# Performance work log

Hardware: AMD Instinct MI355X
Metric: run time of the kernel (lower is better)

## Reference

```python
import jax, jax.numpy as jnp
import numpy as np

EPS = 1e-12


def sage_pool_conv(x, src, dst, W_pool, b_pool, W_self, W_neigh, b, num_nodes):
    """DGL SAGEConv with aggregator_type='pool':
    h_neigh[v] = max_{u in N(v)} relu(x[u] @ W_pool + b_pool)
    out[v] = x[v] @ W_self + h_neigh[v] @ W_neigh + b
    Zero-in-degree nodes get h_neigh = 0 (DGL fills max over empty set with 0).
    """
    m = jax.nn.relu(x[src] @ W_pool + b_pool)            # [E, F] gathered + transformed
    agg = jax.ops.segment_max(m, dst, num_segments=num_nodes)  # [N, F], -inf where no neighbors
    agg = jnp.where(jnp.isneginf(agg), 0.0, agg)
    return x @ W_self + agg @ W_neigh + b


def l2norm_relu(h):
    # F.normalize(h, p=2, dim=1, eps=1e-12) then relu
    n = jnp.maximum(jnp.linalg.norm(h, axis=1, keepdims=True), EPS)
    return jax.nn.relu(h / n)


def setup_inputs() -> dict:
    key = jax.random.key(0)
    N, E = 50000, 1600000
    IN, HID, OUT = 128, 128, 128
    ks = jax.random.split(key, 16)
    s = 0.05
    return {
        "x": jax.random.normal(ks[0], (N, IN), dtype=jnp.float32),
        "src": jax.random.randint(ks[1], (E,), 0, N, dtype=jnp.int32),
        "dst": jax.random.randint(ks[2], (E,), 0, N, dtype=jnp.int32),
        "W_pool1": jax.random.normal(ks[3], (IN, IN), dtype=jnp.float32) * s,
        "b_pool1": jnp.zeros((IN,), dtype=jnp.float32),
        "W_self1": jax.random.normal(ks[4], (IN, HID), dtype=jnp.float32) * s,
        "W_neigh1": jax.random.normal(ks[5], (IN, HID), dtype=jnp.float32) * s,
        "b1": jnp.zeros((HID,), dtype=jnp.float32),
        "W_pool2": jax.random.normal(ks[6], (HID, HID), dtype=jnp.float32) * s,
        "b_pool2": jnp.zeros((HID,), dtype=jnp.float32),
        "W_self2": jax.random.normal(ks[7], (HID, OUT), dtype=jnp.float32) * s,
        "W_neigh2": jax.random.normal(ks[8], (HID, OUT), dtype=jnp.float32) * s,
        "b2": jnp.zeros((OUT,), dtype=jnp.float32),
    }


def reference(x, src, dst, W_pool1, b_pool1, W_self1, W_neigh1, b1,
              W_pool2, b_pool2, W_self2, W_neigh2, b2):
    N = x.shape[0]
    h = sage_pool_conv(x, src, dst, W_pool1, b_pool1, W_self1, W_neigh1, b1, N)
    h = l2norm_relu(h)
    # dropout_1 is re-assigned in the original forward but never applied -> no dropout
    h = sage_pool_conv(h, src, dst, W_pool2, b_pool2, W_self2, W_neigh2, b2, N)
    h = l2norm_relu(h)
    return h
```

## Files before the change

### kernel.cpp

```cpp
#include <hip/hip_runtime.h>
#include <hip/hip_bf16.h>

#define NF 128
#define TILE_B 8192
#define NSLAB 8
#define SLAB_SHIFT 13
#define CSR_CAP 15360

typedef __attribute__((ext_vector_type(8))) short bf8;
typedef __attribute__((ext_vector_type(4))) float f4;
typedef unsigned short u16x8 __attribute__((ext_vector_type(8)));

static __device__ __forceinline__ unsigned short f2bf(float f) {
  unsigned u = __builtin_bit_cast(unsigned, f);
  u = u + 0x7FFF + ((u >> 16) & 1);
  return (unsigned short)(u >> 16);
}

static __device__ __forceinline__ uint4 pkmax4(uint4 a, uint4 b) {
  u16x8 x = __builtin_bit_cast(u16x8, a);
  u16x8 y = __builtin_bit_cast(u16x8, b);
  u16x8 m = __builtin_elementwise_max(x, y);
  return __builtin_bit_cast(uint4, m);
}

static __device__ __forceinline__ uint4 shflxor4(uint4 a, int m) {
  uint4 r;
  r.x = (unsigned)__shfl_xor((int)a.x, m, 64);
  r.y = (unsigned)__shfl_xor((int)a.y, m, 64);
  r.z = (unsigned)__shfl_xor((int)a.z, m, 64);
  r.w = (unsigned)__shfl_xor((int)a.w, m, 64);
  return r;
}


__global__ __launch_bounds__(256) void k_prep(
    const float* __restrict__ x, unsigned short* __restrict__ Xb, long long nelX,
    const int* __restrict__ dst, int* __restrict__ bcnt, int E, int gTile,
    const float* W0, const float* W1, const float* W2,
    const float* W3, const float* W4, const float* W5,
    unsigned short* __restrict__ Wpack) {
  __shared__ int h[256];
  int b = blockIdx.x, tid = threadIdx.x;

  long long i = ((long long)b * 256 + tid) * 8;
  if (i + 8 <= nelX) {
    float4 a = *(const float4*)(x + i);
    float4 c = *(const float4*)(x + i + 4);
    uint4 o;
    o.x = f2bf(a.x) | ((unsigned)f2bf(a.y) << 16);
    o.y = f2bf(a.z) | ((unsigned)f2bf(a.w) << 16);
    o.z = f2bf(c.x) | ((unsigned)f2bf(c.y) << 16);
    o.w = f2bf(c.z) | ((unsigned)f2bf(c.w) << 16);
    *(uint4*)(Xb + i) = o;
  }

  if (b < gTile) {
    h[tid] = 0;
    __syncthreads();
    int t0 = b * TILE_B;
    int tend = min(E, t0 + TILE_B);
    for (int k = t0 + tid; k < tend; k += 256) atomicAdd(&h[dst[k] >> 8], 1);
    __syncthreads();
    if (h[tid] > 0) atomicAdd(&bcnt[tid], h[tid]);
  } else if (b < gTile + 48) {
    int gid = (b - gTile) * 256 + tid;
    int m = gid >> 11;
    int u = gid & 2047;
    const float* W = (m == 0) ? W0 : (m == 1) ? W1 : (m == 2) ? W2
                   : (m == 3) ? W3 : (m == 4) ? W4 : W5;
    int l = u & 63, c = u >> 6;
    int kk = c & 3, t = c >> 2;
    int kb = kk * 32 + ((l >> 4) << 3);
    int n = t * 16 + (l & 15);
    unsigned short* o = Wpack + (size_t)m * 2048 * 8 + (size_t)u * 8;
    #pragma unroll
    for (int j = 0; j < 8; ++j) o[j] = f2bf(W[(size_t)(kb + j) * NF + n]);
  }
}


__global__ __launch_bounds__(256) void k_binB(const int* __restrict__ src,
                                              const int* __restrict__ dst,
                                              const int* __restrict__ bcnt,
                                              int* __restrict__ gcur,
                                              unsigned* __restrict__ tmp, int E) {
  __shared__ int h[256], hs[256], gb[256], lc[256], bo[256];
  __shared__ unsigned sorted[TILE_B];
  int tid = threadIdx.x;
  int t0 = blockIdx.x * TILE_B;
  int tcnt = min(E - t0, TILE_B);
  if (tcnt <= 0) return;

  int bv = bcnt[tid];
  hs[tid] = bv;
  __syncthreads();
  for (int d = 1; d < 256; d <<= 1) {
    int t = (tid >= d) ? hs[tid - d] : 0;
    __syncthreads();
    hs[tid] += t;
    __syncthreads();
  }
  bo[tid] = hs[tid] - bv;
  h[tid] = 0;
  __syncthreads();

  for (int i = tid; i < tcnt; i += 256) atomicAdd(&h[dst[t0 + i] >> 8], 1);
  __syncthreads();
  int v = h[tid];
  hs[tid] = v;
  __syncthreads();
  for (int d = 1; d < 256; d <<= 1) {
    int t = (tid >= d) ? hs[tid - d] : 0;
    __syncthreads();
    hs[tid] += t;
    __syncthreads();
  }
  lc[tid] = 0;
  gb[tid] = bo[tid] + ((v > 0) ? atomicAdd(&gcur[tid], v) : 0);
  __syncthreads();
  for (int i = tid; i < tcnt; i += 256) {
    int d = dst[t0 + i];
    unsigned s = (unsigned)src[t0 + i];
    int b = d >> 8;
    int p = (hs[b] - h[b]) + atomicAdd(&lc[b], 1);
    sorted[p] = ((unsigned)b << 24) | (s << 8) | (unsigned)(d & 255);
  }
  __syncthreads();
  for (int i = tid; i < tcnt; i += 256) {
    unsigned ev = sorted[i];
    int b = ev >> 24;
    tmp[gb[b] + (i - (hs[b] - h[b]))] = ev & 0xFFFFFFu;
  }
}


__global__ __launch_bounds__(256) void k_binC(const unsigned* __restrict__ tmp,
                                              const int* __restrict__ bcnt,
                                              int* __restrict__ off,
                                              unsigned short* __restrict__ esrc,
                                              int N, int E) {
  __shared__ int pre[256 * NSLAB];
  __shared__ int lc2[256 * NSLAB];
  __shared__ int s256[256];
  __shared__ int bo[256];
  __shared__ int csr[CSR_CAP];
  int tid = threadIdx.x;
  int b = blockIdx.x;
  int base = b << 8;

  int bv = bcnt[tid];
  s256[tid] = bv;
  __syncthreads();
  for (int d = 1; d < 256; d <<= 1) {
    int t = (tid >= d) ? s256[tid - d] : 0;
    __syncthreads();
    s256[tid] += t;
    __syncthreads();
  }
  bo[tid] = s256[tid] - bv;
  for (int k = tid; k < 256 * NSLAB; k += 256) { pre[k] = 0; lc2[k] = 0; }
  __syncthreads();

  int beg = bo[b];
  int cnt = bcnt[b];
  int end = beg + cnt;

  for (int i = beg + tid; i < end; i += 256) {
    unsigned e = tmp[i];
    int key = ((e & 255) << 3) | (e >> (8 + SLAB_SHIFT));
    atomicAdd(&pre[key], 1);
  }
  __syncthreads();
  {
    int sum = 0;
    #pragma unroll
    for (int j = 0; j < NSLAB; ++j) {
      int v = pre[tid * NSLAB + j];
      pre[tid * NSLAB + j] = sum;
      sum += v;
    }
    s256[tid] = sum;
    __syncthreads();
    for (int d = 1; d < 256; d <<= 1) {
      int t = (tid >= d) ? s256[tid - d] : 0;
      __syncthreads();
      s256[tid] += t;
      __syncthreads();
    }
    int segbase = s256[tid] - sum;
    #pragma unroll
    for (int j = 0; j < NSLAB; ++j) pre[tid * NSLAB + j] += segbase;
  }
  __syncthreads();

  if (base + tid < N) off[base + tid] = beg + pre[tid * NSLAB];
  if (b == 0 && tid == 0) off[N] = E;

  if (cnt <= CSR_CAP) {
    for (int i = beg + tid; i < end; i += 256) {
      unsigned e = tmp[i];
      int key = ((e & 255) << 3) | (e >> (8 + SLAB_SHIFT));
      int p = pre[key] + atomicAdd(&lc2[key], 1);
      csr[p] = (int)(e >> 8);
    }
    __syncthreads();
    for (int i = tid; i < cnt; i += 256) esrc[beg + i] = (unsigned short)csr[i];
  } else {
    for (int i = beg + tid; i < end; i += 256) {
      unsigned e = tmp[i];
      int key = ((e & 255) << 3) | (e >> (8 + SLAB_SHIFT));
      int p = pre[key] + atomicAdd(&lc2[key], 1);
      esrc[beg + p] = (unsigned short)(e >> 8);
    }
  }
}


__global__ __launch_bounds__(512) void k_gemm_pool(
    const unsigned short* __restrict__ A, const unsigned short* __restrict__ P,
    const float* __restrict__ bias, unsigned short* __restrict__ Yout, int M) {
  __shared__ __align__(16) char smem[32768 + 8 * 4096];
  int tid = threadIdx.x, w = tid >> 6, lane = tid & 63;
  int r0 = lane & 15, g = lane >> 4;

  {
    uint4* S = (uint4*)smem;
    const uint4* Pv = (const uint4*)P;
    for (int t = tid; t < 2048; t += 512) S[t] = Pv[t];
  }
  float bb[8];
  #pragma unroll
  for (int t = 0; t < 8; ++t) bb[t] = bias[t * 16 + r0];
  __syncthreads();

  const bf8* Wl = (const bf8*)smem;
  char* myst = smem + 32768 + w * 4096;

  int T = (M + 15) >> 4;
  int stride = gridDim.x * 8;
  for (int t0i = blockIdx.x * 8 + w; t0i < T; t0i += stride) {
    int rowbase = t0i * 16;
    int arow = min(rowbase + r0, M - 1);

    f4 acc[8];
    #pragma unroll
    for (int t = 0; t < 8; ++t) acc[t] = (f4){0.f, 0.f, 0.f, 0.f};

    const bf8* Ar = (const bf8*)(A + (size_t)arow * NF);
    #pragma unroll
    for (int kk = 0; kk < 4; ++kk) {
      bf8 a = Ar[kk * 4 + g];
      #pragma unroll
      for (int t = 0; t < 8; ++t)
        acc[t] = __builtin_amdgcn_mfma_f32_16x16x32_bf16(a, Wl[(t * 4 + kk) * 64 + lane], acc[t], 0, 0, 0);
    }

    unsigned short* So = (unsigned short*)myst;
    #pragma unroll
    for (int i = 0; i < 4; ++i)
      #pragma unroll
      for (int t = 0; t < 8; ++t)
        So[(g * 4 + i) * NF + t * 16 + r0] = f2bf(fmaxf(acc[t][i] + bb[t], 0.f));
    uint4* Og = (uint4*)(Yout + (size_t)rowbase * NF);
    const uint4* Sv = (const uint4*)myst;
    int maxc = min(16, M - rowbase) * 16;
    #pragma unroll
    for (int k = 0; k < 4; ++k) {
      int c = lane + k * 64;
      if (c < maxc) Og[c] = Sv[c];
    }
  }
}


template <int OUT_MODE>
__global__ __launch_bounds__(256) void k_gemm_dual(
    const unsigned short* __restrict__ A0, const unsigned short* __restrict__ P0,
    const unsigned short* __restrict__ A1, const unsigned short* __restrict__ P1,
    const float* __restrict__ bias, void* __restrict__ Cout, int M) {
  constexpr int STG = (OUT_MODE == 2) ? 8192 : 4096;
  __shared__ __align__(16) char smem[4 * STG];
  int tid = threadIdx.x, w = tid >> 6, lane = tid & 63;
  int r0 = lane & 15, g = lane >> 4;
  int rowbase = (blockIdx.x * 4 + w) * 16;
  if (rowbase >= M) return;
  int arow = min(rowbase + r0, M - 1);
  char* myst = smem + w * STG;

  f4 acc[8];
  #pragma unroll
  for (int t = 0; t < 8; ++t) acc[t] = (f4){0.f, 0.f, 0.f, 0.f};

  #pragma unroll
  for (int mat = 0; mat < 2; ++mat) {
    const unsigned short* A = (mat == 0) ? A0 : A1;
    const bf8* Pp = (const bf8*)((mat == 0) ? P0 : P1);
    const bf8* Ar = (const bf8*)(A + (size_t)arow * NF);
    #pragma unroll
    for (int kk = 0; kk < 4; ++kk) {
      bf8 a = Ar[kk * 4 + g];
      #pragma unroll
      for (int t = 0; t < 8; ++t)
        acc[t] = __builtin_amdgcn_mfma_f32_16x16x32_bf16(a, Pp[(t * 4 + kk) * 64 + lane], acc[t], 0, 0, 0);
    }
  }

  float bb[8];
  #pragma unroll
  for (int t = 0; t < 8; ++t) bb[t] = bias[t * 16 + r0];

  float val[8][4];
  #pragma unroll
  for (int t = 0; t < 8; ++t)
    #pragma unroll
    for (int i = 0; i < 4; ++i) val[t][i] = acc[t][i] + bb[t];

  float ss[4] = {0.f, 0.f, 0.f, 0.f};
  #pragma unroll
  for (int i = 0; i < 4; ++i)
    #pragma unroll
    for (int t = 0; t < 8; ++t) ss[i] += val[t][i] * val[t][i];
  #pragma unroll
  for (int d = 1; d < 16; d <<= 1)
    #pragma unroll
    for (int i = 0; i < 4; ++i) ss[i] += __shfl_xor(ss[i], d, 64);
  float inv[4];
  #pragma unroll
  for (int i = 0; i < 4; ++i) inv[i] = 1.f / fmaxf(sqrtf(ss[i]), 1e-12f);

  int maxrows = min(16, M - rowbase);
  if (OUT_MODE == 2) {
    float* So = (float*)myst;
    #pragma unroll
    for (int i = 0; i < 4; ++i)
      #pragma unroll
      for (int t = 0; t < 8; ++t)
        So[(g * 4 + i) * NF + t * 16 + r0] = fmaxf(val[t][i] * inv[i], 0.f);
    uint4* Og = (uint4*)((float*)Cout + (size_t)rowbase * NF);
    const uint4* Sv = (const uint4*)myst;
    int maxc = maxrows * 32;
    #pragma unroll
    for (int k = 0; k < 8; ++k) {
      int c = lane + k * 64;
      if (c < maxc) Og[c] = Sv[c];
    }
  } else {
    unsigned short* So = (unsigned short*)myst;
    #pragma unroll
    for (int i = 0; i < 4; ++i)
      #pragma unroll
      for (int t = 0; t < 8; ++t)
        So[(g * 4 + i) * NF + t * 16 + r0] = f2bf(fmaxf(val[t][i] * inv[i], 0.f));
    uint4* Og = (uint4*)((unsigned short*)Cout + (size_t)rowbase * NF);
    const uint4* Sv = (const uint4*)myst;
    int maxc = maxrows * 16;
    #pragma unroll
    for (int k = 0; k < 4; ++k) {
      int c = lane + k * 64;
      if (c < maxc) Og[c] = Sv[c];
    }
  }
}


__global__ __launch_bounds__(256) void k_gather_max(
    const unsigned short* __restrict__ Y, const int* __restrict__ off,
    const unsigned short* __restrict__ esrc, unsigned short* __restrict__ AGG, int N) {
  int w = (blockIdx.x * 256 + threadIdx.x) >> 6;
  int lane = threadIdx.x & 63;
  if (w >= N) return;
  int r0 = lane & 15, g = lane >> 4;
  int s = __builtin_amdgcn_readfirstlane(off[w]);
  int e = __builtin_amdgcn_readfirstlane(off[w + 1]);
  uint4 am[4];
  #pragma unroll
  for (int j = 0; j < 4; ++j) am[j] = (uint4){0u, 0u, 0u, 0u};
  for (int b0 = s; b0 < e; b0 += 64) {
    int cnt = min(64, e - b0);
    int idxv = (int)esrc[b0 + min(lane, cnt - 1)];
    for (int i = 0; i < cnt; i += 16) {
      #pragma unroll
      for (int j = 0; j < 4; ++j) {
        int eo = min(i + j * 4 + g, cnt - 1);
        int u = __shfl(idxv, eo, 64);
        uint4 v = *((const uint4*)(Y + (size_t)u * NF) + r0);
        am[j] = pkmax4(am[j], v);
      }
    }
  }
  uint4 a01 = pkmax4(am[0], am[1]);
  uint4 a23 = pkmax4(am[2], am[3]);
  uint4 a = pkmax4(a01, a23);
  a = pkmax4(a, shflxor4(a, 16));
  a = pkmax4(a, shflxor4(a, 32));
  if (g == 0) *(uint4*)(AGG + (size_t)w * NF + r0 * 8) = a;
}


extern "C" void kernel_launch(void* const* d_in, const int* in_sizes, int n_in,
                              void* d_out, int out_size, void* d_ws, size_t ws_size,
                              hipStream_t stream) {
  const float* x   = (const float*)d_in[0];
  const int*   src = (const int*)d_in[1];
  const int*   dst = (const int*)d_in[2];
  const float* Wp1 = (const float*)d_in[3];
  const float* bp1 = (const float*)d_in[4];
  const float* Ws1 = (const float*)d_in[5];
  const float* Wn1 = (const float*)d_in[6];
  const float* b1  = (const float*)d_in[7];
  const float* Wp2 = (const float*)d_in[8];
  const float* bp2 = (const float*)d_in[9];
  const float* Ws2 = (const float*)d_in[10];
  const float* Wn2 = (const float*)d_in[11];
  const float* b2  = (const float*)d_in[12];
  float* out = (float*)d_out;

  const int N = in_sizes[0] / NF;
  const int E = in_sizes[1];

  char* ws = (char*)d_ws;
  auto carve = [&](size_t bytes) { char* p = ws; ws += (bytes + 255) & ~(size_t)255; return p; };
  unsigned short* Xb    = (unsigned short*)carve((size_t)N * NF * 2);
  unsigned short* Yb    = (unsigned short*)carve((size_t)N * NF * 2);
  unsigned short* AGGb  = (unsigned short*)carve((size_t)N * NF * 2);
  unsigned short* Hb    = (unsigned short*)carve((size_t)N * NF * 2);
  unsigned short* Wpack = (unsigned short*)carve((size_t)6 * NF * NF * 2);
  int* off     = (int*)carve((size_t)(N + 1) * 4);
  int* meta    = (int*)carve(512 * 4);
  unsigned* tmp = (unsigned*)carve((size_t)E * 4);
  unsigned short* esrc = (unsigned short*)carve((size_t)E * 2);

  int* bcnt = meta;
  int* gcur = meta + 256;

  unsigned short* Pp1 = Wpack + 0 * NF * NF;
  unsigned short* Ps1 = Wpack + 1 * NF * NF;
  unsigned short* Pn1 = Wpack + 2 * NF * NF;
  unsigned short* Pp2 = Wpack + 3 * NF * NF;
  unsigned short* Ps2 = Wpack + 4 * NF * NF;
  unsigned short* Pn2 = Wpack + 5 * NF * NF;

  const long long nelX = (long long)N * NF;
  const int gConv = (int)((nelX / 8 + 255) / 256);
  const int gTile = (E + TILE_B - 1) / TILE_B;
  const int NB    = (N + 255) >> 8;
  const int gRW   = (N + 3) / 4;
  const int gDual = (((N + 15) >> 4) + 3) / 4;

  hipMemsetAsync(meta, 0, 512 * 4, stream);
  k_prep<<<gConv, 256, 0, stream>>>(x, Xb, nelX, dst, bcnt, E, gTile,
                                    Wp1, Ws1, Wn1, Wp2, Ws2, Wn2, Wpack);
  k_binB<<<gTile, 256, 0, stream>>>(src, dst, bcnt, gcur, tmp, E);
  k_binC<<<NB, 256, 0, stream>>>(tmp, bcnt, off, esrc, N, E);

  k_gemm_pool<<<512, 512, 0, stream>>>(Xb, Pp1, bp1, Yb, N);
  k_gather_max<<<gRW, 256, 0, stream>>>(Yb, off, esrc, AGGb, N);
  k_gemm_dual<1><<<gDual, 256, 0, stream>>>(Xb, Ps1, AGGb, Pn1, b1, Hb, N);

  k_gemm_pool<<<512, 512, 0, stream>>>(Hb, Pp2, bp2, Yb, N);
  k_gather_max<<<gRW, 256, 0, stream>>>(Yb, off, esrc, AGGb, N);
  k_gemm_dual<2><<<gDual, 256, 0, stream>>>(Hb, Ps2, AGGb, Pn2, b2, out, N);
}
```

Measured before the change: 308.6 us.

## Fuse pool GEMMs into binning and dual kernels, simplify CSR bucket sort

The layer-1 pool GEMM is split across extra blocks appended to the two binning kernels, so it runs concurrently with the edge sort instead of as its own launch. The layer-1 dual GEMM plus normalize is fused with the layer-2 pool GEMM, which reuses the normalized H tile from shared memory and avoids re-reading Hb. The per-bucket CSR construction drops the 8-slab sub-sort for a plain per-destination counting sort. Risks include larger shared-memory footprints lowering occupancy, uneven block work within the heterogeneous grids, and a change in the neighbor order within each destination, which does not affect the max.

```diff
diff --git a/kernel.cpp b/kernel.cpp
--- a/kernel.cpp
+++ b/kernel.cpp
@@ -3,8 +3,6 @@
 
 #define NF 128
 #define TILE_B 8192
-#define NSLAB 8
-#define SLAB_SHIFT 13
 #define CSR_CAP 15360
 
 typedef __attribute__((ext_vector_type(8))) short bf8;
@@ -80,17 +78,72 @@
 }
 
 
-__global__ __launch_bounds__(256) void k_binB(const int* __restrict__ src,
-                                              const int* __restrict__ dst,
-                                              const int* __restrict__ bcnt,
-                                              int* __restrict__ gcur,
-                                              unsigned* __restrict__ tmp, int E) {
-  __shared__ int h[256], hs[256], gb[256], lc[256], bo[256];
-  __shared__ unsigned sorted[TILE_B];
+static __device__ __forceinline__ void pool_body(
+    char* smem, int tile,
+    const unsigned short* __restrict__ A, const unsigned short* __restrict__ P,
+    const float* __restrict__ bias, unsigned short* __restrict__ Yout, int M) {
+  int tid = threadIdx.x, w = tid >> 6, lane = tid & 63;
+  int r0 = lane & 15, g = lane >> 4;
+  {
+    uint4* S = (uint4*)smem;
+    const uint4* Pv = (const uint4*)P;
+    for (int t = tid; t < 2048; t += 256) S[t] = Pv[t];
+  }
+  float bb[8];
+  #pragma unroll
+  for (int t = 0; t < 8; ++t) bb[t] = bias[t * 16 + r0];
+  __syncthreads();
+
+  int base = tile * 64;
+  int arow = min(base + w * 16 + r0, M - 1);
+  f4 acc[8];
+  #pragma unroll
+  for (int t = 0; t < 8; ++t) acc[t] = (f4){0.f, 0.f, 0.f, 0.f};
+  const bf8* Ar = (const bf8*)(A + (size_t)arow * NF);
+  const bf8* Wl = (const bf8*)smem;
+  #pragma unroll
+  for (int kk = 0; kk < 4; ++kk) {
+    bf8 a = Ar[kk * 4 + g];
+    #pragma unroll
+    for (int t = 0; t < 8; ++t)
+      acc[t] = __builtin_amdgcn_mfma_f32_16x16x32_bf16(a, Wl[(t * 4 + kk) * 64 + lane], acc[t], 0, 0, 0);
+  }
+  __syncthreads();
+  unsigned short* So = (unsigned short*)smem;
+  #pragma unroll
+  for (int i = 0; i < 4; ++i)
+    #pragma unroll
+    for (int t = 0; t < 8; ++t)
+      So[(w * 16 + g * 4 + i) * NF + t * 16 + r0] = f2bf(fmaxf(acc[t][i] + bb[t], 0.f));
+  __syncthreads();
+  int maxc = min(64, M - base) * 16;
+  uint4* Og = (uint4*)(Yout + (size_t)base * NF);
+  const uint4* Sv = (const uint4*)smem;
+  for (int c = tid; c < 1024; c += 256)
+    if (c < maxc) Og[c] = Sv[c];
+}
+
+
+__global__ __launch_bounds__(256) void k_binB_pool(
+    const int* __restrict__ src, const int* __restrict__ dst,
+    const int* __restrict__ bcnt, int* __restrict__ gcur,
+    unsigned* __restrict__ tmp, int E, int gTile,
+    const unsigned short* __restrict__ A, const unsigned short* __restrict__ P,
+    const float* __restrict__ bias, unsigned short* __restrict__ Yout, int M) {
+  __shared__ __align__(16) char smem[37888];
+  int b = blockIdx.x;
+  if (b >= gTile) { pool_body(smem, b - gTile, A, P, bias, Yout, M); return; }
+
   int tid = threadIdx.x;
-  int t0 = blockIdx.x * TILE_B;
+  int* h  = (int*)smem;
+  int* hs = h + 256;
+  int* gb = hs + 256;
+  int* lc = gb + 256;
+  int* bo = lc + 256;
+  unsigned* sorted = (unsigned*)(bo + 256);
+
+  int t0 = b * TILE_B;
   int tcnt = min(E - t0, TILE_B);
-  if (tcnt <= 0) return;
 
   int bv = bcnt[tid];
   hs[tid] = bv;
@@ -122,31 +175,35 @@
   for (int i = tid; i < tcnt; i += 256) {
     int d = dst[t0 + i];
     unsigned s = (unsigned)src[t0 + i];
-    int b = d >> 8;
-    int p = (hs[b] - h[b]) + atomicAdd(&lc[b], 1);
-    sorted[p] = ((unsigned)b << 24) | (s << 8) | (unsigned)(d & 255);
+    int bk = d >> 8;
+    int p = (hs[bk] - h[bk]) + atomicAdd(&lc[bk], 1);
+    sorted[p] = ((unsigned)bk << 24) | (s << 8) | (unsigned)(d & 255);
   }
   __syncthreads();
   for (int i = tid; i < tcnt; i += 256) {
     unsigned ev = sorted[i];
-    int b = ev >> 24;
-    tmp[gb[b] + (i - (hs[b] - h[b]))] = ev & 0xFFFFFFu;
-  }
-}
-
-
-__global__ __launch_bounds__(256) void k_binC(const unsigned* __restrict__ tmp,
-                                              const int* __restrict__ bcnt,
-                                              int* __restrict__ off,
-                                              unsigned short* __restrict__ esrc,
-                                              int N, int E) {
-  __shared__ int pre[256 * NSLAB];
-  __shared__ int lc2[256 * NSLAB];
-  __shared__ int s256[256];
-  __shared__ int bo[256];
-  __shared__ int csr[CSR_CAP];
+    int bk = ev >> 24;
+    tmp[gb[bk] + (i - (hs[bk] - h[bk]))] = ev & 0xFFFFFFu;
+  }
+}
+
+
+__global__ __launch_bounds__(256) void k_binC_pool(
+    const unsigned* __restrict__ tmp, const int* __restrict__ bcnt,
+    int* __restrict__ off, unsigned short* __restrict__ esrc, int N, int E, int NB,
+    const unsigned short* __restrict__ A, const unsigned short* __restrict__ P,
+    const float* __restrict__ bias, unsigned short* __restrict__ Yout, int M, int tileOff) {
+  __shared__ __align__(16) char smem[66560];
+  int b = blockIdx.x;
+  if (b >= NB) { pool_body(smem, tileOff + b - NB, A, P, bias, Yout, M); return; }
+
   int tid = threadIdx.x;
-  int b = blockIdx.x;
+  int* s256 = (int*)smem;
+  int* bo   = s256 + 256;
+  int* lh   = bo + 256;
+  int* ls   = lh + 256;
+  int* lcur = ls + 256;
+  int* csr  = lcur + 256;
   int base = b << 8;
 
   int bv = bcnt[tid];
@@ -159,49 +216,34 @@
     __syncthreads();
   }
   bo[tid] = s256[tid] - bv;
-  for (int k = tid; k < 256 * NSLAB; k += 256) { pre[k] = 0; lc2[k] = 0; }
+  lh[tid] = 0;
   __syncthreads();
 
   int beg = bo[b];
   int cnt = bcnt[b];
   int end = beg + cnt;
 
-  for (int i = beg + tid; i < end; i += 256) {
-    unsigned e = tmp[i];
-    int key = ((e & 255) << 3) | (e >> (8 + SLAB_SHIFT));
-    atomicAdd(&pre[key], 1);
-  }
-  __syncthreads();
-  {
-    int sum = 0;
-    #pragma unroll
-    for (int j = 0; j < NSLAB; ++j) {
-      int v = pre[tid * NSLAB + j];
-      pre[tid * NSLAB + j] = sum;
-      sum += v;
-    }
-    s256[tid] = sum;
-    __syncthreads();
-    for (int d = 1; d < 256; d <<= 1) {
-      int t = (tid >= d) ? s256[tid - d] : 0;
-      __syncthreads();
-      s256[tid] += t;
-      __syncthreads();
-    }
-    int segbase = s256[tid] - sum;
-    #pragma unroll
-    for (int j = 0; j < NSLAB; ++j) pre[tid * NSLAB + j] += segbase;
-  }
-  __syncthreads();
-
-  if (base + tid < N) off[base + tid] = beg + pre[tid * NSLAB];
+  for (int i = beg + tid; i < end; i += 256) atomicAdd(&lh[tmp[i] & 255], 1);
+  __syncthreads();
+  int v = lh[tid];
+  ls[tid] = v;
+  __syncthreads();
+  for (int d = 1; d < 256; d <<= 1) {
+    int t = (tid >= d) ? ls[tid - d] : 0;
+    __syncthreads();
+    ls[tid] += t;
+    __syncthreads();
+  }
+  if (base + tid < N) off[base + tid] = beg + (ls[tid] - v);
   if (b == 0 && tid == 0) off[N] = E;
+  lcur[tid] = 0;
+  __syncthreads();
 
   if (cnt <= CSR_CAP) {
     for (int i = beg + tid; i < end; i += 256) {
       unsigned e = tmp[i];
-      int key = ((e & 255) << 3) | (e >> (8 + SLAB_SHIFT));
-      int p = pre[key] + atomicAdd(&lc2[key], 1);
+      int dl = (int)(e & 255);
+      int p = (ls[dl] - lh[dl]) + atomicAdd(&lcur[dl], 1);
       csr[p] = (int)(e >> 8);
     }
     __syncthreads();
@@ -209,156 +251,9 @@
   } else {
     for (int i = beg + tid; i < end; i += 256) {
       unsigned e = tmp[i];
-      int key = ((e & 255) << 3) | (e >> (8 + SLAB_SHIFT));
-      int p = pre[key] + atomicAdd(&lc2[key], 1);
+      int dl = (int)(e & 255);
+      int p = (ls[dl] - lh[dl]) + atomicAdd(&lcur[dl], 1);
       esrc[beg + p] = (unsigned short)(e >> 8);
-    }
-  }
-}
-
-
-__global__ __launch_bounds__(512) void k_gemm_pool(
-    const unsigned short* __restrict__ A, const unsigned short* __restrict__ P,
-    const float* __restrict__ bias, unsigned short* __restrict__ Yout, int M) {
-  __shared__ __align__(16) char smem[32768 + 8 * 4096];
-  int tid = threadIdx.x, w = tid >> 6, lane = tid & 63;
-  int r0 = lane & 15, g = lane >> 4;
-
-  {
-    uint4* S = (uint4*)smem;
-    const uint4* Pv = (const uint4*)P;
-    for (int t = tid; t < 2048; t += 512) S[t] = Pv[t];
-  }
-  float bb[8];
-  #pragma unroll
-  for (int t = 0; t < 8; ++t) bb[t] = bias[t * 16 + r0];
-  __syncthreads();
-
-  const bf8* Wl = (const bf8*)smem;
-  char* myst = smem + 32768 + w * 4096;
-
-  int T = (M + 15) >> 4;
-  int stride = gridDim.x * 8;
-  for (int t0i = blockIdx.x * 8 + w; t0i < T; t0i += stride) {
-    int rowbase = t0i * 16;
-    int arow = min(rowbase + r0, M - 1);
-
-    f4 acc[8];
-    #pragma unroll
-    for (int t = 0; t < 8; ++t) acc[t] = (f4){0.f, 0.f, 0.f, 0.f};
-
-    const bf8* Ar = (const bf8*)(A + (size_t)arow * NF);
-    #pragma unroll
-    for (int kk = 0; kk < 4; ++kk) {
-      bf8 a = Ar[kk * 4 + g];
-      #pragma unroll
-      for (int t = 0; t < 8; ++t)
-        acc[t] = __builtin_amdgcn_mfma_f32_16x16x32_bf16(a, Wl[(t * 4 + kk) * 64 + lane], acc[t], 0, 0, 0);
-    }
-
-    unsigned short* So = (unsigned short*)myst;
-    #pragma unroll
-    for (int i = 0; i < 4; ++i)
-      #pragma unroll
-      for (int t = 0; t < 8; ++t)
-        So[(g * 4 + i) * NF + t * 16 + r0] = f2bf(fmaxf(acc[t][i] + bb[t], 0.f));
-    uint4* Og = (uint4*)(Yout + (size_t)rowbase * NF);
-    const uint4* Sv = (const uint4*)myst;
-    int maxc = min(16, M - rowbase) * 16;
-    #pragma unroll
-    for (int k = 0; k < 4; ++k) {
-      int c = lane + k * 64;
-      if (c < maxc) Og[c] = Sv[c];
-    }
-  }
-}
-
-
-template <int OUT_MODE>
-__global__ __launch_bounds__(256) void k_gemm_dual(
-    const unsigned short* __restrict__ A0, const unsigned short* __restrict__ P0,
-    const unsigned short* __restrict__ A1, const unsigned short* __restrict__ P1,
-    const float* __restrict__ bias, void* __restrict__ Cout, int M) {
-  constexpr int STG = (OUT_MODE == 2) ? 8192 : 4096;
-  __shared__ __align__(16) char smem[4 * STG];
-  int tid = threadIdx.x, w = tid >> 6, lane = tid & 63;
-  int r0 = lane & 15, g = lane >> 4;
-  int rowbase = (blockIdx.x * 4 + w) * 16;
-  if (rowbase >= M) return;
-  int arow = min(rowbase + r0, M - 1);
-  char* myst = smem + w * STG;
-
-  f4 acc[8];
-  #pragma unroll
-  for (int t = 0; t < 8; ++t) acc[t] = (f4){0.f, 0.f, 0.f, 0.f};
-
-  #pragma unroll
-  for (int mat = 0; mat < 2; ++mat) {
-    const unsigned short* A = (mat == 0) ? A0 : A1;
-    const bf8* Pp = (const bf8*)((mat == 0) ? P0 : P1);
-    const bf8* Ar = (const bf8*)(A + (size_t)arow * NF);
-    #pragma unroll
-    for (int kk = 0; kk < 4; ++kk) {
-      bf8 a = Ar[kk * 4 + g];
-      #pragma unroll
-      for (int t = 0; t < 8; ++t)
-        acc[t] = __builtin_amdgcn_mfma_f32_16x16x32_bf16(a, Pp[(t * 4 + kk) * 64 + lane], acc[t], 0, 0, 0);
-    }
-  }
-
-  float bb[8];
-  #pragma unroll
-  for (int t = 0; t < 8; ++t) bb[t] = bias[t * 16 + r0];
-
-  float val[8][4];
-  #pragma unroll
-  for (int t = 0; t < 8; ++t)
-    #pragma unroll
-    for (int i = 0; i < 4; ++i) val[t][i] = acc[t][i] + bb[t];
-
-  float ss[4] = {0.f, 0.f, 0.f, 0.f};
-  #pragma unroll
-  for (int i = 0; i < 4; ++i)
-    #pragma unroll
-    for (int t = 0; t < 8; ++t) ss[i] += val[t][i] * val[t][i];
-  #pragma unroll
-  for (int d = 1; d < 16; d <<= 1)
-    #pragma unroll
-    for (int i = 0; i < 4; ++i) ss[i] += __shfl_xor(ss[i], d, 64);
-  float inv[4];
-  #pragma unroll
-  for (int i = 0; i < 4; ++i) inv[i] = 1.f / fmaxf(sqrtf(ss[i]), 1e-12f);
-
-  int maxrows = min(16, M - rowbase);
-  if (OUT_MODE == 2) {
-    float* So = (float*)myst;
-    #pragma unroll
-    for (int i = 0; i < 4; ++i)
-      #pragma unroll
-      for (int t = 0; t < 8; ++t)
-        So[(g * 4 + i) * NF + t * 16 + r0] = fmaxf(val[t][i] * inv[i], 0.f);
-    uint4* Og = (uint4*)((float*)Cout + (size_t)rowbase * NF);
-    const uint4* Sv = (const uint4*)myst;
-    int maxc = maxrows * 32;
-    #pragma unroll
-    for (int k = 0; k < 8; ++k) {
-      int c = lane + k * 64;
-      if (c < maxc) Og[c] = Sv[c];
-    }
-  } else {
-    unsigned short* So = (unsigned short*)myst;
-    #pragma unroll
-    for (int i = 0; i < 4; ++i)
-      #pragma unroll
-      for (int t = 0; t < 8; ++t)
-        So[(g * 4 + i) * NF + t * 16 + r0] = f2bf(fmaxf(val[t][i] * inv[i], 0.f));
-    uint4* Og = (uint4*)((unsigned short*)Cout + (size_t)rowbase * NF);
-    const uint4* Sv = (const uint4*)myst;
-    int maxc = maxrows * 16;
-    #pragma unroll
-    for (int k = 0; k < 4; ++k) {
-      int c = lane + k * 64;
-      if (c < maxc) Og[c] = Sv[c];
     }
   }
 }
@@ -395,6 +290,192 @@
   a = pkmax4(a, shflxor4(a, 16));
   a = pkmax4(a, shflxor4(a, 32));
   if (g == 0) *(uint4*)(AGG + (size_t)w * NF + r0 * 8) = a;
+}
+
+
+__global__ __launch_bounds__(256) void k_dual_pool(
+    const unsigned short* __restrict__ Xb, const unsigned short* __restrict__ Ps,
+    const unsigned short* __restrict__ AGG, const unsigned short* __restrict__ Pn,
+    const float* __restrict__ b1,
+    const unsigned short* __restrict__ Pp2, const float* __restrict__ bp2,
+    unsigned short* __restrict__ Hb, unsigned short* __restrict__ Yb, int M) {
+  __shared__ __align__(16) char smem[65536];
+  int tid = threadIdx.x, w = tid >> 6, lane = tid & 63;
+  int r0 = lane & 15, g = lane >> 4;
+  int base = blockIdx.x * 64;
+  int arow = min(base + w * 16 + r0, M - 1);
+  int maxrows = min(64, M - base);
+
+  {
+    uint4* S = (uint4*)smem;
+    const uint4* Pv0 = (const uint4*)Ps;
+    const uint4* Pv1 = (const uint4*)Pn;
+    for (int t = tid; t < 2048; t += 256) S[t] = Pv0[t];
+    for (int t = tid; t < 2048; t += 256) S[2048 + t] = Pv1[t];
+  }
+  float bb[8], bb2[8];
+  #pragma unroll
+  for (int t = 0; t < 8; ++t) { bb[t] = b1[t * 16 + r0]; bb2[t] = bp2[t * 16 + r0]; }
+  __syncthreads();
+
+  f4 acc[8];
+  #pragma unroll
+  for (int t = 0; t < 8; ++t) acc[t] = (f4){0.f, 0.f, 0.f, 0.f};
+  #pragma unroll
+  for (int mat = 0; mat < 2; ++mat) {
+    const unsigned short* A = (mat == 0) ? Xb : AGG;
+    const bf8* Ar = (const bf8*)(A + (size_t)arow * NF);
+    const bf8* Wl = (const bf8*)smem + (size_t)mat * 2048;
+    #pragma unroll
+    for (int kk = 0; kk < 4; ++kk) {
+      bf8 a = Ar[kk * 4 + g];
+      #pragma unroll
+      for (int t = 0; t < 8; ++t)
+        acc[t] = __builtin_amdgcn_mfma_f32_16x16x32_bf16(a, Wl[(t * 4 + kk) * 64 + lane], acc[t], 0, 0, 0);
+    }
+  }
+
+  float val[8][4];
+  #pragma unroll
+  for (int t = 0; t < 8; ++t)
+    #pragma unroll
+    for (int i = 0; i < 4; ++i) val[t][i] = acc[t][i] + bb[t];
+  float ss[4] = {0.f, 0.f, 0.f, 0.f};
+  #pragma unroll
+  for (int i = 0; i < 4; ++i)
+    #pragma unroll
+    for (int t = 0; t < 8; ++t) ss[i] += val[t][i] * val[t][i];
+  #pragma unroll
+  for (int d = 1; d < 16; d <<= 1)
+    #pragma unroll
+    for (int i = 0; i < 4; ++i) ss[i] += __shfl_xor(ss[i], d, 64);
+  float inv[4];
+  #pragma unroll
+  for (int i = 0; i < 4; ++i) inv[i] = 1.f / fmaxf(sqrtf(ss[i]), 1e-12f);
+
+  __syncthreads();
+  unsigned short* So = (unsigned short*)smem;
+  #pragma unroll
+  for (int i = 0; i < 4; ++i)
+    #pragma unroll
+    for (int t = 0; t < 8; ++t)
+      So[(w * 16 + g * 4 + i) * 136 + t * 16 + r0] = f2bf(fmaxf(val[t][i] * inv[i], 0.f));
+  __syncthreads();
+
+  {
+    uint4* Og = (uint4*)(Hb + (size_t)base * NF);
+    for (int c = tid; c < 1024; c += 256) {
+      int row = c >> 4, ch = c & 15;
+      if (row < maxrows) Og[c] = *(const uint4*)(So + row * 136 + ch * 8);
+    }
+  }
+  bf8 hfrag[4];
+  #pragma unroll
+  for (int kk = 0; kk < 4; ++kk)
+    hfrag[kk] = *(const bf8*)(So + (w * 16 + r0) * 136 + kk * 32 + g * 8);
+  {
+    uint4* S2 = (uint4*)(smem + 17408);
+    const uint4* Pv2 = (const uint4*)Pp2;
+    for (int t = tid; t < 2048; t += 256) S2[t] = Pv2[t];
+  }
+  __syncthreads();
+
+  #pragma unroll
+  for (int t = 0; t < 8; ++t) acc[t] = (f4){0.f, 0.f, 0.f, 0.f};
+  const bf8* W2 = (const bf8*)(smem + 17408);
+  #pragma unroll
+  for (int kk = 0; kk < 4; ++kk) {
+    #pragma unroll
+    for (int t = 0; t < 8; ++t)
+      acc[t] = __builtin_amdgcn_mfma_f32_16x16x32_bf16(hfrag[kk], W2[(t * 4 + kk) * 64 + lane], acc[t], 0, 0, 0);
+  }
+  #pragma unroll
+  for (int i = 0; i < 4; ++i)
+    #pragma unroll
+    for (int t = 0; t < 8; ++t)
+      So[(w * 16 + g * 4 + i) * 136 + t * 16 + r0] = f2bf(fmaxf(acc[t][i] + bb2[t], 0.f));
+  __syncthreads();
+  {
+    uint4* Og = (uint4*)(Yb + (size_t)base * NF);
+    for (int c = tid; c < 1024; c += 256) {
+      int row = c >> 4, ch = c & 15;
+      if (row < maxrows) Og[c] = *(const uint4*)(So + row * 136 + ch * 8);
+    }
+  }
+}
+
+
+__global__ __launch_bounds__(256) void k_dual_out(
+    const unsigned short* __restrict__ A0, const unsigned short* __restrict__ P0,
+    const unsigned short* __restrict__ A1, const unsigned short* __restrict__ P1,
+    const float* __restrict__ bias, float* __restrict__ Cout, int M) {
+  __shared__ __align__(16) char smem[65536];
+  int tid = threadIdx.x, w = tid >> 6, lane = tid & 63;
+  int r0 = lane & 15, g = lane >> 4;
+  int base = blockIdx.x * 64;
+  int arow = min(base + w * 16 + r0, M - 1);
+
+  {
+    uint4* S = (uint4*)smem;
+    const uint4* Pv0 = (const uint4*)P0;
+    const uint4* Pv1 = (const uint4*)P1;
+    for (int t = tid; t < 2048; t += 256) S[t] = Pv0[t];
+    for (int t = tid; t < 2048; t += 256) S[2048 + t] = Pv1[t];
+  }
+  __syncthreads();
+
+  f4 acc[8];
+  #pragma unroll
+  for (int t = 0; t < 8; ++t) acc[t] = (f4){0.f, 0.f, 0.f, 0.f};
+  #pragma unroll
+  for (int mat = 0; mat < 2; ++mat) {
+    const unsigned short* A = (mat == 0) ? A0 : A1;
+    const bf8* Ar = (const bf8*)(A + (size_t)arow * NF);
+    const bf8* Wl = (const bf8*)smem + (size_t)mat * 2048;
+    #pragma unroll
+    for (int kk = 0; kk < 4; ++kk) {
+      bf8 a = Ar[kk * 4 + g];
+      #pragma unroll
+      for (int t = 0; t < 8; ++t)
+        acc[t] = __builtin_amdgcn_mfma_f32_16x16x32_bf16(a, Wl[(t * 4 + kk) * 64 + lane], acc[t], 0, 0, 0);
+    }
+  }
+
+  float bb[8];
+  #pragma unroll
+  for (int t = 0; t < 8; ++t) bb[t] = bias[t * 16 + r0];
+  float val[8][4];
+  #pragma unroll
+  for (int t = 0; t < 8; ++t)
+    #pragma unroll
+    for (int i = 0; i < 4; ++i) val[t][i] = acc[t][i] + bb[t];
+  float ss[4] = {0.f, 0.f, 0.f, 0.f};
+  #pragma unroll
+  for (int i = 0; i < 4; ++i)
+    #pragma unroll
+    for (int t = 0; t < 8; ++t) ss[i] += val[t][i] * val[t][i];
+  #pragma unroll
+  for (int d = 1; d < 16; d <<= 1)
+    #pragma unroll
+    for (int i = 0; i < 4; ++i) ss[i] += __shfl_xor(ss[i], d, 64);
+  float inv[4];
+  #pragma unroll
+  for (int i = 0; i < 4; ++i) inv[i] = 1.f / fmaxf(sqrtf(ss[i]), 1e-12f);
+
+  __syncthreads();
+  int maxrows = min(64, M - base);
+  float* So = (float*)smem;
+  #pragma unroll
+  for (int i = 0; i < 4; ++i)
+    #pragma unroll
+    for (int t = 0; t < 8; ++t)
+      So[(w * 16 + g * 4 + i) * NF + t * 16 + r0] = fmaxf(val[t][i] * inv[i], 0.f);
+  __syncthreads();
+  uint4* Og = (uint4*)(Cout + (size_t)base * NF);
+  const uint4* Sv = (const uint4*)smem;
+  int maxc = maxrows * 32;
+  for (int c = tid; c < 2048; c += 256)
+    if (c < maxc) Og[c] = Sv[c];
 }
 
 
@@ -446,19 +527,20 @@
   const int gTile = (E + TILE_B - 1) / TILE_B;
   const int NB    = (N + 255) >> 8;
   const int gRW   = (N + 3) / 4;
-  const int gDual = (((N + 15) >> 4) + 3) / 4;
+  const int T     = (N + 63) / 64;
+  const int Thalf = T / 2;
 
   hipMemsetAsync(meta, 0, 512 * 4, stream);
   k_prep<<<gConv, 256, 0, stream>>>(x, Xb, nelX, dst, bcnt, E, gTile,
                                     Wp1, Ws1, Wn1, Wp2, Ws2, Wn2, Wpack);
-  k_binB<<<gTile, 256, 0, stream>>>(src, dst, bcnt, gcur, tmp, E);
-  k_binC<<<NB, 256, 0, stream>>>(tmp, bcnt, off, esrc, N, E);
-
-  k_gemm_pool<<<512, 512, 0, stream>>>(Xb, Pp1, bp1, Yb, N);
+  k_binB_pool<<<gTile + Thalf, 256, 0, stream>>>(src, dst, bcnt, gcur, tmp, E, gTile,
+                                                 Xb, Pp1, bp1, Yb, N);
+  k_binC_pool<<<NB + (T - Thalf), 256, 0, stream>>>(tmp, bcnt, off, esrc, N, E, NB,
+                                                    Xb, Pp1, bp1, Yb, N, Thalf);
+
   k_gather_max<<<gRW, 256, 0, stream>>>(Yb, off, esrc, AGGb, N);
-  k_gemm_dual<1><<<gDual, 256, 0, stream>>>(Xb, Ps1, AGGb, Pn1, b1, Hb, N);
-
-  k_gemm_pool<<<512, 512, 0, stream>>>(Hb, Pp2, bp2, Yb, N);
+  k_dual_pool<<<T, 256, 0, stream>>>(Xb, Ps1, AGGb, Pn1, b1, Pp2, bp2, Hb, Yb, N);
+
   k_gather_max<<<gRW, 256, 0, stream>>>(Yb, off, esrc, AGGb, N);
-  k_gemm_dual<2><<<gDual, 256, 0, stream>>>(Hb, Ps2, AGGb, Pn2, b2, out, N);
-}
+  k_dual_out<<<T, 256, 0, stream>>>(Hb, Ps2, AGGb, Pn2, b2, out, N);
+}
```

Result: faster. 281.3 us (-8.9%).
